# Performance work log

Measured on AMD Instinct MI355X. Metric: run time of the kernel, lower is better.

## Reference

```python
import jax, jax.numpy as jnp
import numpy as np
from jax import lax

B, T, D, H = 64, 2048, 256, 256


def setup_inputs() -> dict:
    key = jax.random.key(0)
    k1, k2, k3 = jax.random.split(key, 3)
    xs = jax.random.normal(k1, (B, T, D), dtype=jnp.float32)
    # scale weights ~ 1/sqrt(fan_in) to keep tanh out of saturation
    W_ih = jax.random.normal(k2, (D, H), dtype=jnp.float32) / np.sqrt(D)
    W_hh = jax.random.normal(k3, (H, H), dtype=jnp.float32) / np.sqrt(H)
    b_hh = jnp.zeros((H,), dtype=jnp.float32)
    c = jnp.zeros((B, H), dtype=jnp.float32)
    return {"c": c, "xs": xs, "W_ih": W_ih, "W_hh": W_hh, "b_hh": b_hh}


def reference(c, xs, W_ih, W_hh, b_hh):
    # Elman RNN: h_t = tanh(x_t @ W_ih + h_{t-1} @ W_hh + b_hh)
    # (the ih bias is created but never applied in the original module)
    # Precompute the input projection for all timesteps in one big GEMM.
    px = jnp.einsum('btd,dh->bth', xs, W_ih)  # [B, T, H]

    def step(h, px_t):
        h_new = jnp.tanh(h @ W_hh + b_hh + px_t)
        return h_new, h_new

    h_final, ys = lax.scan(step, c, px.transpose(1, 0, 2))  # ys: [T, B, H]
    return h_final, ys.transpose(1, 0, 2)  # carry [B,H], outputs [B,T,H]
```

## Files before the change

kernel.cpp:

```cpp
#include <hip/hip_runtime.h>


typedef _Float16 half8 __attribute__((ext_vector_type(8)));
typedef float floatx4 __attribute__((ext_vector_type(4)));
typedef float f32x4 __attribute__((ext_vector_type(4)));

constexpr int Bb = 64, Tt = 2048, Dd = 256, Hh = 256;

__device__ __forceinline__ int lds_addr(int row, int col) {
    return row * 512 + ((((col >> 3) ^ (row & 7)) & 31) << 4) + ((col & 7) << 1);
}

__device__ __forceinline__ float fast_tanh(float x) {
    float e = __builtin_amdgcn_exp2f(x * 2.885390081777927f);
    float r = __builtin_amdgcn_rcpf(e + 1.0f);
    return __builtin_fmaf(-2.0f, r, 1.0f);
}

__global__ __launch_bounds__(256, 2) void px_gemm(const float* __restrict__ xs,
                                                  const float* __restrict__ Wih,
                                                  const float* __restrict__ bhh,
                                                  float* __restrict__ px) {
    const int lane = threadIdx.x & 63;
    const int w = threadIdx.x >> 6;
    const int q = lane >> 4;
    const int m = lane & 15;

    half8 bf[4][8];
#pragma unroll
    for (int tt = 0; tt < 4; ++tt) {
        const int n = 64 * w + 16 * tt + m;
#pragma unroll
        for (int c = 0; c < 8; ++c) {
            half8 f;
#pragma unroll
            for (int j = 0; j < 8; ++j)
                f[j] = (_Float16)Wih[(32 * c + 8 * q + j) * Hh + n];
            bf[tt][c] = f;
        }
    }
    float bias[4];
#pragma unroll
    for (int tt = 0; tt < 4; ++tt) bias[tt] = bhh[64 * w + 16 * tt + m];

    for (int i = 0; i < 8; ++i) {
        const int tau = blockIdx.x * 8 + i;
        const float* arow = xs + (size_t)(tau * 16 + m) * Dd;
        half8 af[8];
#pragma unroll
        for (int c = 0; c < 8; ++c) {
            f32x4 lo = *(const f32x4*)(arow + 32 * c + 8 * q);
            f32x4 hi = *(const f32x4*)(arow + 32 * c + 8 * q + 4);
            half8 f;
            f[0] = (_Float16)lo[0]; f[1] = (_Float16)lo[1];
            f[2] = (_Float16)lo[2]; f[3] = (_Float16)lo[3];
            f[4] = (_Float16)hi[0]; f[5] = (_Float16)hi[1];
            f[6] = (_Float16)hi[2]; f[7] = (_Float16)hi[3];
            af[c] = f;
        }
        floatx4 acc[4];
#pragma unroll
        for (int tt = 0; tt < 4; ++tt) {
            acc[tt][0] = bias[tt]; acc[tt][1] = bias[tt];
            acc[tt][2] = bias[tt]; acc[tt][3] = bias[tt];
        }
#pragma unroll
        for (int c = 0; c < 8; ++c)
#pragma unroll
            for (int tt = 0; tt < 4; ++tt)
                acc[tt] = __builtin_amdgcn_mfma_f32_16x16x32_f16(af[c], bf[tt][c], acc[tt], 0, 0, 0);
#pragma unroll
        for (int tt = 0; tt < 4; ++tt)
#pragma unroll
            for (int r = 0; r < 4; ++r)
                px[(size_t)(tau * 16 + 4 * q + r) * Hh + 64 * w + 16 * tt + m] = acc[tt][r];
    }
}

__global__ __launch_bounds__(512, 1) void rnn_scan(const float* __restrict__ c0,
                                                   const float* __restrict__ Whh,
                                                   float* __restrict__ hfin,
                                                   float* __restrict__ ys) {
    __shared__ alignas(16) unsigned char hb[2][8192];
    const int g = blockIdx.x;
    const int lane = threadIdx.x & 63;
    const int w = threadIdx.x >> 6;
    const int q = lane >> 4;
    const int m = lane & 15;

    half8 bf[2][8];
#pragma unroll
    for (int tt = 0; tt < 2; ++tt) {
        const int n = 32 * w + 16 * tt + m;
#pragma unroll
        for (int c = 0; c < 8; ++c) {
            half8 f;
#pragma unroll
            for (int j = 0; j < 8; ++j)
                f[j] = (_Float16)Whh[(32 * c + 8 * q + j) * Hh + n];
            bf[tt][c] = f;
        }
    }

    for (int i = threadIdx.x; i < 16 * 256; i += 512) {
        const int row = i >> 8, col = i & 255;
        *(_Float16*)&hb[0][lds_addr(row, col)] = (_Float16)c0[(16 * g + row) * Hh + col];
    }

    size_t rowoff[4];
#pragma unroll
    for (int r = 0; r < 4; ++r)
        rowoff[r] = (size_t)(16 * g + 4 * q + r) * Tt * Hh;
    int coloff[2];
    coloff[0] = 32 * w + m;
    coloff[1] = 32 * w + 16 + m;

    float pxc[8], pxn[8];
#pragma unroll
    for (int tt = 0; tt < 2; ++tt)
#pragma unroll
        for (int r = 0; r < 4; ++r)
            pxc[4 * tt + r] = ys[rowoff[r] + coloff[tt]];

    __syncthreads();

    for (int t = 0; t < Tt; ++t) {
        const int p = t & 1;
        const int tn = (t + 1 < Tt) ? t + 1 : t;
#pragma unroll
        for (int tt = 0; tt < 2; ++tt)
#pragma unroll
            for (int r = 0; r < 4; ++r)
                pxn[4 * tt + r] = ys[rowoff[r] + (size_t)tn * Hh + coloff[tt]];

        half8 af[8];
#pragma unroll
        for (int c = 0; c < 8; ++c)
            af[c] = *(const half8*)&hb[p][m * 512 + ((((4 * c + q) ^ (m & 7)) & 31) << 4)];

        floatx4 acc[2];
#pragma unroll
        for (int tt = 0; tt < 2; ++tt) {
            acc[tt][0] = pxc[4 * tt + 0]; acc[tt][1] = pxc[4 * tt + 1];
            acc[tt][2] = pxc[4 * tt + 2]; acc[tt][3] = pxc[4 * tt + 3];
        }
#pragma unroll
        for (int tt = 0; tt < 2; ++tt)
#pragma unroll
            for (int c = 0; c < 8; ++c)
                acc[tt] = __builtin_amdgcn_mfma_f32_16x16x32_f16(af[c], bf[tt][c], acc[tt], 0, 0, 0);

#pragma unroll
        for (int tt = 0; tt < 2; ++tt) {
#pragma unroll
            for (int r = 0; r < 4; ++r) {
                const float h = fast_tanh(acc[tt][r]);
                const int row = 4 * q + r;
                const int col = coloff[tt];
                ys[rowoff[r] + (size_t)t * Hh + col] = h;
                *(_Float16*)&hb[p ^ 1][lds_addr(row, col)] = (_Float16)h;
                if (t == Tt - 1) hfin[(16 * g + row) * Hh + col] = h;
            }
        }
#pragma unroll
        for (int k = 0; k < 8; ++k) pxc[k] = pxn[k];
        __syncthreads();
    }
}

extern "C" void kernel_launch(void* const* d_in, const int* in_sizes, int n_in,
                              void* d_out, int out_size, void* d_ws, size_t ws_size,
                              hipStream_t stream) {
    const float* c0  = (const float*)d_in[0];
    const float* xs  = (const float*)d_in[1];
    const float* Wih = (const float*)d_in[2];
    const float* Whh = (const float*)d_in[3];
    const float* bhh = (const float*)d_in[4];
    float* out = (float*)d_out;
    float* hfin = out;
    float* ys = out + Bb * Hh;

    px_gemm<<<1024, 256, 0, stream>>>(xs, Wih, bhh, ys);
    rnn_scan<<<Bb / 16, 512, 0, stream>>>(c0, Whh, hfin, ys);
}
```

Measured before the change: 1.768 ms.

## Halve scan block to 4 waves, 64 columns per wave, unroll by two

The recurrent scan kernel now runs 4 waves per block instead of 8, so each wave computes 64 hidden columns (4 MFMA tiles) rather than 32. The time loop is manually unrolled by two, swapping the double-buffered px registers without copies, and all global and LDS addresses are precomputed as byte offsets. The aim is to make the per-step barrier cheaper and cut address arithmetic on the serial critical path. In exchange each wave holds twice as many W_hh fragments in registers and issues a longer MFMA chain per step.

```diff
diff --git a/kernel.cpp b/kernel.cpp
--- a/kernel.cpp
+++ b/kernel.cpp
@@ -77,7 +77,7 @@
     }
 }
 
-__global__ __launch_bounds__(512, 1) void rnn_scan(const float* __restrict__ c0,
+__global__ __launch_bounds__(256, 1) void rnn_scan(const float* __restrict__ c0,
                                                    const float* __restrict__ Whh,
                                                    float* __restrict__ hfin,
                                                    float* __restrict__ ys) {
@@ -88,10 +88,10 @@
     const int q = lane >> 4;
     const int m = lane & 15;
 
-    half8 bf[2][8];
+    half8 bf[4][8];
 #pragma unroll
-    for (int tt = 0; tt < 2; ++tt) {
-        const int n = 32 * w + 16 * tt + m;
+    for (int tt = 0; tt < 4; ++tt) {
+        const int n = 64 * w + 16 * tt + m;
 #pragma unroll
         for (int c = 0; c < 8; ++c) {
             half8 f;
@@ -102,70 +102,78 @@
         }
     }
 
-    for (int i = threadIdx.x; i < 16 * 256; i += 512) {
+    for (int i = threadIdx.x; i < 16 * 256; i += 256) {
         const int row = i >> 8, col = i & 255;
         *(_Float16*)&hb[0][lds_addr(row, col)] = (_Float16)c0[(16 * g + row) * Hh + col];
     }
 
-    size_t rowoff[4];
+    unsigned boff[16];
 #pragma unroll
-    for (int r = 0; r < 4; ++r)
-        rowoff[r] = (size_t)(16 * g + 4 * q + r) * Tt * Hh;
-    int coloff[2];
-    coloff[0] = 32 * w + m;
-    coloff[1] = 32 * w + 16 + m;
-
-    float pxc[8], pxn[8];
-#pragma unroll
-    for (int tt = 0; tt < 2; ++tt)
+    for (int tt = 0; tt < 4; ++tt)
 #pragma unroll
         for (int r = 0; r < 4; ++r)
-            pxc[4 * tt + r] = ys[rowoff[r] + coloff[tt]];
+            boff[4 * tt + r] =
+                (unsigned)(((16 * g + 4 * q + r) * Tt) * Hh + 64 * w + 16 * tt + m) * 4u;
+
+    int ard[8];
+#pragma unroll
+    for (int c = 0; c < 8; ++c)
+        ard[c] = m * 512 + ((((4 * c + q) ^ (m & 7)) & 31) << 4);
+
+    int wad[16];
+#pragma unroll
+    for (int tt = 0; tt < 4; ++tt)
+#pragma unroll
+        for (int r = 0; r < 4; ++r)
+            wad[4 * tt + r] = lds_addr(4 * q + r, 64 * w + 16 * tt + m);
+
+    const char* pxp = (const char*)ys;
+    const char* pxlast = (const char*)ys + (size_t)(Tt - 1) * Hh * 4;
+    char* yst = (char*)ys;
+
+    float pxA[16], pxB[16];
+#pragma unroll
+    for (int k = 0; k < 16; ++k) pxA[k] = *(const float*)(pxp + boff[k]);
+    pxp += Hh * 4;
 
     __syncthreads();
 
-    for (int t = 0; t < Tt; ++t) {
-        const int p = t & 1;
-        const int tn = (t + 1 < Tt) ? t + 1 : t;
-#pragma unroll
-        for (int tt = 0; tt < 2; ++tt)
-#pragma unroll
-            for (int r = 0; r < 4; ++r)
-                pxn[4 * tt + r] = ys[rowoff[r] + (size_t)tn * Hh + coloff[tt]];
+#define RNN_STEP(P, PXC, PXN, LASTCHK, TCUR)                                   \
+    {                                                                          \
+        const char* pf = (pxp > pxlast) ? pxlast : pxp;     \
+        _Pragma("unroll") for (int k2 = 0; k2 < 16; ++k2)                      \
+            PXN[k2] = *(const float*)(pf + boff[k2]);                          \
+        pxp += Hh * 4;                                                         \
+        half8 af[8];                                                           \
+        _Pragma("unroll") for (int c2 = 0; c2 < 8; ++c2)                       \
+            af[c2] = *(const half8*)&hb[(P)][ard[c2]];                         \
+        floatx4 acc[4];                                                        \
+        _Pragma("unroll") for (int u2 = 0; u2 < 4; ++u2) {                     \
+            acc[u2][0] = PXC[4 * u2 + 0]; acc[u2][1] = PXC[4 * u2 + 1];        \
+            acc[u2][2] = PXC[4 * u2 + 2]; acc[u2][3] = PXC[4 * u2 + 3];        \
+        }                                                                      \
+                        \
+        _Pragma("unroll") for (int c2 = 0; c2 < 8; ++c2)                       \
+            _Pragma("unroll") for (int u2 = 0; u2 < 4; ++u2)                   \
+                acc[u2] = __builtin_amdgcn_mfma_f32_16x16x32_f16(              \
+                    af[c2], bf[u2][c2], acc[u2], 0, 0, 0);                     \
+        _Pragma("unroll") for (int u2 = 0; u2 < 4; ++u2)                       \
+            _Pragma("unroll") for (int r2 = 0; r2 < 4; ++r2) {                 \
+                const float hv = fast_tanh(acc[u2][r2]);                       \
+                *(float*)(yst + boff[4 * u2 + r2]) = hv;                       \
+                *(_Float16*)&hb[(P) ^ 1][wad[4 * u2 + r2]] = (_Float16)hv;     \
+                if ((LASTCHK) && (TCUR) == Tt - 1)                             \
+                    hfin[(16 * g + 4 * q + r2) * Hh + 64 * w + 16 * u2 + m] = hv; \
+            }                                                                  \
+        yst += Hh * 4;                                                         \
+        __syncthreads();                                                       \
+    }
 
-        half8 af[8];
-#pragma unroll
-        for (int c = 0; c < 8; ++c)
-            af[c] = *(const half8*)&hb[p][m * 512 + ((((4 * c + q) ^ (m & 7)) & 31) << 4)];
-
-        floatx4 acc[2];
-#pragma unroll
-        for (int tt = 0; tt < 2; ++tt) {
-            acc[tt][0] = pxc[4 * tt + 0]; acc[tt][1] = pxc[4 * tt + 1];
-            acc[tt][2] = pxc[4 * tt + 2]; acc[tt][3] = pxc[4 * tt + 3];
-        }
-#pragma unroll
-        for (int tt = 0; tt < 2; ++tt)
-#pragma unroll
-            for (int c = 0; c < 8; ++c)
-                acc[tt] = __builtin_amdgcn_mfma_f32_16x16x32_f16(af[c], bf[tt][c], acc[tt], 0, 0, 0);
-
-#pragma unroll
-        for (int tt = 0; tt < 2; ++tt) {
-#pragma unroll
-            for (int r = 0; r < 4; ++r) {
-                const float h = fast_tanh(acc[tt][r]);
-                const int row = 4 * q + r;
-                const int col = coloff[tt];
-                ys[rowoff[r] + (size_t)t * Hh + col] = h;
-                *(_Float16*)&hb[p ^ 1][lds_addr(row, col)] = (_Float16)h;
-                if (t == Tt - 1) hfin[(16 * g + row) * Hh + col] = h;
-            }
-        }
-#pragma unroll
-        for (int k = 0; k < 8; ++k) pxc[k] = pxn[k];
-        __syncthreads();
+    for (int t = 0; t < Tt; t += 2) {
+        RNN_STEP(0, pxA, pxB, 0, t)
+        RNN_STEP(1, pxB, pxA, 1, t + 1)
     }
+#undef RNN_STEP
 }
 
 extern "C" void kernel_launch(void* const* d_in, const int* in_sizes, int n_in,
@@ -181,5 +189,5 @@
     float* ys = out + Bb * Hh;
 
     px_gemm<<<1024, 256, 0, stream>>>(xs, Wih, bhh, ys);
-    rnn_scan<<<Bb / 16, 512, 0, stream>>>(c0, Whh, hfin, ys);
+    rnn_scan<<<Bb / 16, 256, 0, stream>>>(c0, Whh, hfin, ys);
 }
```

After: 2.423 ms. +37.0%, slower.
